# Kernel optimization log

Hardware: AMD Instinct MI355X
Metric: run time of the kernel (lower is better)

## Reference

```python
import jax, jax.numpy as jnp
import numpy as np

B, S, E, H = 4096, 200, 64, 128
V_U0, V_U1, V_I = 100000, 1000, 1000000

def setup_inputs() -> dict:
    key = jax.random.key(0)
    ks = jax.random.split(key, 16)
    s = 0.05
    return {
        'user_features': jax.random.randint(ks[0], (B, 2), 0, V_U1, dtype=jnp.int32),
        'target_item_features': jax.random.randint(ks[1], (B, 1), 0, V_I, dtype=jnp.int32),
        'behavior_sequence': jax.random.randint(ks[2], (B, S, 1), 0, V_I, dtype=jnp.int32),
        'emb_user0': jax.random.normal(ks[3], (V_U0, E), jnp.float32) * s,
        'emb_user1': jax.random.normal(ks[4], (V_U1, E), jnp.float32) * s,
        'emb_item': jax.random.normal(ks[5], (V_I, E), jnp.float32) * s,
        'att_w1': jax.random.normal(ks[6], (4 * E, H), jnp.float32) * s,
        'att_b1': jnp.zeros((H,), jnp.float32),
        'att_w2': jax.random.normal(ks[7], (H, 1), jnp.float32) * s,
        'att_b2': jnp.zeros((1,), jnp.float32),
        'fc_w1': jax.random.normal(ks[8], (4 * E, H), jnp.float32) * s,
        'fc_b1': jnp.zeros((H,), jnp.float32),
        'fc_w2': jax.random.normal(ks[9], (H, 1), jnp.float32) * s,
        'fc_b2': jnp.zeros((1,), jnp.float32),
    }

def reference(user_features, target_item_features, behavior_sequence,
              emb_user0, emb_user1, emb_item,
              att_w1, att_b1, att_w2, att_b2,
              fc_w1, fc_b1, fc_w2, fc_b2):
    # embedding gathers
    user_embeds = jnp.concatenate([emb_user0[user_features[:, 0]],
                                   emb_user1[user_features[:, 1]]], axis=-1)  # [B, 2E]
    target = emb_item[target_item_features[:, 0]]                              # [B, E]
    behavior = emb_item[behavior_sequence[:, :, 0]]                            # [B, S, E]
    t = target[:, None, :]                                                     # [B, 1, E]
    t_exp = jnp.broadcast_to(t, behavior.shape)
    att_in = jnp.concatenate([behavior, t_exp, behavior - t, behavior * t], axis=-1)  # [B, S, 4E]
    # attention MLP -> scores
    h = jax.nn.relu(jnp.einsum('bsd,dh->bsh', att_in, att_w1) + att_b1)
    scores = (jnp.einsum('bsh,ho->bso', h, att_w2) + att_b2)[..., 0]           # [B, S]
    weights = jax.nn.softmax(scores, axis=1)
    user_interest = jnp.einsum('bse,bs->be', behavior, weights)                # [B, E]
    combined = jnp.concatenate([user_embeds, user_interest, target], axis=-1)  # [B, 4E]
    out = jax.nn.relu(combined @ fc_w1 + fc_b1) @ fc_w2 + fc_b2                # [B, 1]
    return out
```

## Files before the change

### kernel.cpp

```cpp
#include <hip/hip_runtime.h>
#include <math.h>


#define S_LEN 200
#define S_PAD 208

typedef __attribute__((ext_vector_type(8))) short short8;
typedef __attribute__((ext_vector_type(4))) float f32x4;

__device__ __forceinline__ unsigned short f2b(float f) {
  union { float f; unsigned u; } x; x.f = f;
  unsigned r = x.u + 0x7fffu + ((x.u >> 16) & 1u);
  return (unsigned short)(r >> 16);
}
__device__ __forceinline__ float b2f(unsigned short h) {
  union { unsigned u; float f; } x; x.u = ((unsigned)h) << 16; return x.f;
}
__device__ __forceinline__ unsigned cvt_pk_bf16(float lo, float hi) {
  unsigned r;
  asm("v_cvt_pk_bf16_f32 %0, %1, %2" : "=v"(r) : "v"(lo), "v"(hi));
  return r;
}

__device__ __forceinline__ int swzB(int row, int col) {
  int byte = row * 128 + col * 2;
  byte ^= (row & 7) << 4;
  return byte >> 1;
}
__device__ __forceinline__ int swzW(int row, int col) {
  int byte = row * 512 + col * 2;
  byte ^= (row & 7) << 4;
  return byte >> 1;
}

__device__ __forceinline__ void async_g2l_16(const void* g, void* l) {
  __builtin_amdgcn_global_load_lds(
      (const __attribute__((address_space(1))) void*)g,
      (__attribute__((address_space(3))) void*)l, 16, 0, 0);
}

template <int CTRL>
__device__ __forceinline__ float dpp_add(float v) {
  const int t = __builtin_amdgcn_mov_dpp(__float_as_int(v), CTRL, 0xF, 0xF, true);
  return v + __int_as_float(t);
}
__device__ __forceinline__ float rowReduce16(float v) {
  v = dpp_add<0xB1>(v);
  v = dpp_add<0x4E>(v);
  v = dpp_add<0x124>(v);
  v = dpp_add<0x128>(v);
  return v;
}
__device__ __forceinline__ float permAdd16(float p) {
  float a = p, b = p;
  asm("v_permlane16_swap_b32 %0, %1" : "+v"(a), "+v"(b));
  return a + b;
}
__device__ __forceinline__ float permAdd32(float p) {
  float a = p, b = p;
  asm("v_permlane32_swap_b32 %0, %1" : "+v"(a), "+v"(b));
  return a + b;
}
__device__ __forceinline__ float waveSum64(float v) {
  return permAdd32(permAdd16(rowReduce16(v)));
}

#define WS_COMB 0
#define WS_AT   2097152
#define WS_DT   2113536
#define WS_BM   2129920
#define WS_FW1T 2146304

__global__ __launch_bounds__(256)
void din_prep(const float* __restrict__ aw1, const float* __restrict__ fw1,
              char* __restrict__ ws)
{
  unsigned short* ATc  = (unsigned short*)(ws + WS_AT);
  unsigned short* DTc  = (unsigned short*)(ws + WS_DT);
  unsigned short* BMc  = (unsigned short*)(ws + WS_BM);
  unsigned short* FW1T = (unsigned short*)(ws + WS_FW1T);
  const int blk = blockIdx.x, tid = threadIdx.x;

  if (blk < 64) {
    const int i = (blk & 31) * 256 + tid;
    const int h = i >> 6, d = i & 63;
    const int hg = h >> 5, ht = (h >> 4) & 1, hl = h & 15;
    const int kk = d >> 5, rq = (d >> 3) & 3, j = d & 7;
    const int o = (hg * 2 + ht) * 1024 + kk * 512 + rq * 128 + hl * 8 + j;
    if (blk < 32) {
      const float a  = aw1[d * 128 + h];
      const float c  = aw1[(128 + d) * 128 + h];
      const float dd = aw1[(192 + d) * 128 + h];
      ATc[o] = f2b(a + c);
      DTc[o] = f2b(dd);
    } else {
      BMc[o] = f2b(aw1[(64 + d) * 128 + h] - aw1[(128 + d) * 128 + h]);
    }
  } else {
    const int i = (blk - 64) * 256 + tid;
    const int o = 2 * i;
    const int h = o >> 9;
    const int rr = o & 511;
    const int d = (rr ^ ((h & 7) << 4)) >> 1;
    FW1T[i] = f2b(fw1[d * 128 + h]);
  }
}

__global__ __launch_bounds__(256, 4)
void din_main(const int* __restrict__ uf, const int* __restrict__ tif,
              const int* __restrict__ bseq,
              const float* __restrict__ e0, const float* __restrict__ e1,
              const float* __restrict__ ei,
              const float* __restrict__ ab1, const float* __restrict__ aw2,
              char* __restrict__ ws)
{
  __shared__ unsigned short sBeh[13312];
  __shared__ float sPart[4][S_PAD];
  __shared__ float sScores[S_PAD];
  __shared__ float sPool[4][64];
  __shared__ float sRedS[4];

  unsigned short* combS = (unsigned short*)(ws + WS_COMB);
  const unsigned short* ATc = (const unsigned short*)(ws + WS_AT);
  const unsigned short* DTc = (const unsigned short*)(ws + WS_DT);
  const unsigned short* BMc = (const unsigned short*)(ws + WS_BM);

  const int b    = blockIdx.x;
  const int tid  = threadIdx.x;
  const int lane = tid & 63;
  const int wv   = tid >> 6;
  const int hl   = lane & 15;
  const int rq   = lane >> 4;

  const int ti = tif[b];

  float4 gv[13];
#pragma unroll
  for (int it = 0; it < 13; ++it) {
    const int row = it * 16 + (tid >> 4);
    if (row < S_LEN) {
      const int idx = bseq[b * S_LEN + row];
      gv[it] = *(const float4*)(ei + (size_t)idx * 64 + (tid & 15) * 4);
    }
  }
  const float* trow = ei + (size_t)ti * 64;
  const float4 tx0 = *(const float4*)(trow + rq * 8);
  const float4 tx1 = *(const float4*)(trow + rq * 8 + 4);
  const float4 ty0 = *(const float4*)(trow + 32 + rq * 8);
  const float4 ty1 = *(const float4*)(trow + 32 + rq * 8 + 4);
  __builtin_amdgcn_sched_barrier(0);

  if (tid < 128) {
    const int row = 200 + (tid >> 4), c = (tid & 15) * 4;
    ushort4 z = {0, 0, 0, 0};
    *(ushort4*)&sBeh[swzB(row, c)] = z;
  }

  {
    unsigned short* ct = combS + (size_t)(b >> 4) * 4096;
    const int row = b & 15;
    if (tid < 64) {
      const int u0 = uf[2 * b];
      ct[swzW(row, tid)] = f2b(e0[(size_t)u0 * 64 + tid]);
    } else if (tid < 128) {
      const int u1 = uf[2 * b + 1];
      ct[swzW(row, 64 + (tid - 64))] = f2b(e1[(size_t)u1 * 64 + (tid - 64)]);
    } else if (tid < 192) {
      ct[swzW(row, 192 + (tid - 128))] = f2b(trow[tid - 128]);
    }
  }

  const float4 w2v0 = *(const float4*)(aw2 + wv * 32 + rq * 4);
  const float4 w2v1 = *(const float4*)(aw2 + wv * 32 + 16 + rq * 4);
  const f32x4 abv0 = *(const f32x4*)(ab1 + wv * 32 + rq * 4);
  const f32x4 abv1 = *(const f32x4*)(ab1 + wv * 32 + 16 + rq * 4);

  const float tt0[8] = {tx0.x, tx0.y, tx0.z, tx0.w, tx1.x, tx1.y, tx1.z, tx1.w};
  const float tt1[8] = {ty0.x, ty0.y, ty0.z, ty0.w, ty1.x, ty1.y, ty1.z, ty1.w};
  short8 w[2][2];
#pragma unroll
  for (int ht = 0; ht < 2; ++ht) {
#pragma unroll
    for (int kk = 0; kk < 2; ++kk) {
      const int fo = (wv * 2 + ht) * 1024 + kk * 512 + lane * 8;
      const short8 a8 = *(const short8*)(ATc + fo);
      const short8 d8 = *(const short8*)(DTc + fo);
      const float* tk = kk ? tt1 : tt0;
      union { short8 s; unsigned u[4]; } o;
#pragma unroll
      for (int p = 0; p < 4; ++p) {
        const float lo = fmaf(tk[2*p],   b2f((unsigned short)d8[2*p]),   b2f((unsigned short)a8[2*p]));
        const float hi = fmaf(tk[2*p+1], b2f((unsigned short)d8[2*p+1]), b2f((unsigned short)a8[2*p+1]));
        o.u[p] = cvt_pk_bf16(lo, hi);
      }
      w[ht][kk] = o.s;
    }
  }
  short8 ttB0, ttB1;
  {
    union { short8 s; unsigned u[4]; } o;
#pragma unroll
    for (int p = 0; p < 4; ++p) o.u[p] = cvt_pk_bf16(tt0[2*p], tt0[2*p+1]);
    ttB0 = o.s;
#pragma unroll
    for (int p = 0; p < 4; ++p) o.u[p] = cvt_pk_bf16(tt1[2*p], tt1[2*p+1]);
    ttB1 = o.s;
  }

#pragma unroll
  for (int it = 0; it < 13; ++it) {
    const int row = it * 16 + (tid >> 4);
    if (row < S_LEN) {
      const float4 v = gv[it];
      uint2 pk;
      pk.x = cvt_pk_bf16(v.x, v.y);
      pk.y = cvt_pk_bf16(v.z, v.w);
      *(uint2*)&sBeh[swzB(row, (tid & 15) * 4)] = pk;
    }
  }

  f32x4 accInit0, accInit1;
  {
    const f32x4 z = {0.f, 0.f, 0.f, 0.f};
    f32x4 c0 = z, c1 = z;
    const short8 bm00 = *(const short8*)(BMc + (wv * 2) * 1024 + lane * 8);
    const short8 bm01 = *(const short8*)(BMc + (wv * 2) * 1024 + 512 + lane * 8);
    const short8 bm10 = *(const short8*)(BMc + (wv * 2 + 1) * 1024 + lane * 8);
    const short8 bm11 = *(const short8*)(BMc + (wv * 2 + 1) * 1024 + 512 + lane * 8);
    c0 = __builtin_amdgcn_mfma_f32_16x16x32_bf16(bm00, ttB0, c0, 0, 0, 0);
    c0 = __builtin_amdgcn_mfma_f32_16x16x32_bf16(bm01, ttB1, c0, 0, 0, 0);
    c1 = __builtin_amdgcn_mfma_f32_16x16x32_bf16(bm10, ttB0, c1, 0, 0, 0);
    c1 = __builtin_amdgcn_mfma_f32_16x16x32_bf16(bm11, ttB1, c1, 0, 0, 0);
#pragma unroll
    for (int r = 0; r < 4; ++r) {
      accInit0[r] = c0[r] + abv0[r];
      accInit1[r] = c1[r] + abv1[r];
    }
  }
  __syncthreads();

#pragma unroll 2
  for (int tile = 0; tile < 13; ++tile) {
    const short8 av0 = *(const short8*)&sBeh[swzB(tile * 16 + hl, rq * 8)];
    const short8 av1 = *(const short8*)&sBeh[swzB(tile * 16 + hl, 32 + rq * 8)];
    f32x4 acc = accInit0;
    acc = __builtin_amdgcn_mfma_f32_16x16x32_bf16(w[0][0], av0, acc, 0, 0, 0);
    acc = __builtin_amdgcn_mfma_f32_16x16x32_bf16(w[0][1], av1, acc, 0, 0, 0);
    float p;
    p = fmaxf(acc[0], 0.f) * w2v0.x;
    p = fmaf(fmaxf(acc[1], 0.f), w2v0.y, p);
    p = fmaf(fmaxf(acc[2], 0.f), w2v0.z, p);
    p = fmaf(fmaxf(acc[3], 0.f), w2v0.w, p);
    f32x4 acc2 = accInit1;
    acc2 = __builtin_amdgcn_mfma_f32_16x16x32_bf16(w[1][0], av0, acc2, 0, 0, 0);
    acc2 = __builtin_amdgcn_mfma_f32_16x16x32_bf16(w[1][1], av1, acc2, 0, 0, 0);
    p = fmaf(fmaxf(acc2[0], 0.f), w2v1.x, p);
    p = fmaf(fmaxf(acc2[1], 0.f), w2v1.y, p);
    p = fmaf(fmaxf(acc2[2], 0.f), w2v1.z, p);
    p = fmaf(fmaxf(acc2[3], 0.f), w2v1.w, p);
    p = permAdd32(permAdd16(p));
    if (lane < 16) sPart[wv][tile * 16 + lane] = p;
  }
  __syncthreads();

  float e = 0.f;
  if (tid < S_PAD) {
    if (tid < S_LEN)
      e = __expf((sPart[0][tid] + sPart[1][tid]) + (sPart[2][tid] + sPart[3][tid]));
    sScores[tid] = e;
  }
  {
    const float s = waveSum64(e);
    if (lane == 0) sRedS[wv] = s;
  }
  __syncthreads();

  const float invS = 1.f / (sRedS[0] + sRedS[1] + sRedS[2] + sRedS[3]);

  {
    const int e2 = lane & 31, rr = lane >> 5;
    float p0 = 0.f, p1 = 0.f;
#pragma unroll
    for (int k = 0; k < 13; ++k) {
      const int base = 16 * k + 4 * wv + 2 * rr;
      const float2 sc2 = *(const float2*)&sScores[base];
      const unsigned u0 = *(const unsigned*)&sBeh[swzB(base, e2 * 2)];
      p0 = fmaf(sc2.x, __int_as_float((int)(u0 << 16)), p0);
      p1 = fmaf(sc2.x, __int_as_float((int)(u0 & 0xffff0000u)), p1);
      const unsigned u1 = *(const unsigned*)&sBeh[swzB(base + 1, e2 * 2)];
      p0 = fmaf(sc2.y, __int_as_float((int)(u1 << 16)), p0);
      p1 = fmaf(sc2.y, __int_as_float((int)(u1 & 0xffff0000u)), p1);
    }
    p0 = permAdd32(p0);
    p1 = permAdd32(p1);
    if (lane < 32) {
      float2 pr; pr.x = p0; pr.y = p1;
      *(float2*)&sPool[wv][e2 * 2] = pr;
    }
  }
  __syncthreads();

  if (tid < 64) {
    const float a = sPool[0][tid] + sPool[1][tid] + sPool[2][tid] + sPool[3][tid];
    combS[(size_t)(b >> 4) * 4096 + swzW(b & 15, 128 + tid)] = f2b(a * invS);
  }
}

__global__ __launch_bounds__(256, 2)
void din_fc(const float* __restrict__ fb1, const float* __restrict__ fw2,
            const float* __restrict__ fb2, const char* __restrict__ ws,
            float* __restrict__ out)
{
  __shared__ unsigned short sW[32768];
  __shared__ unsigned short sA[4096];
  __shared__ float sO[64];

  const int tid  = threadIdx.x;
  const int lane = tid & 63;
  const int wv   = tid >> 6;
  const int bb   = blockIdx.x * 16;

  {
    const char* srcW = ws + WS_FW1T;
    char* dstW = (char*)sW;
#pragma unroll
    for (int it = 0; it < 16; ++it)
      async_g2l_16(srcW + it * 4096 + tid * 16, dstW + it * 4096 + tid * 16);
    const char* srcA = ws + WS_COMB + (size_t)blockIdx.x * 8192;
    char* dstA = (char*)sA;
    async_g2l_16(srcA + tid * 16, dstA + tid * 16);
    async_g2l_16(srcA + 4096 + tid * 16, dstA + 4096 + tid * 16);
  }
  __syncthreads();

  const int hl = lane & 15, rq = lane >> 4;
  const int h0 = wv * 32 + hl, h1 = h0 + 16;
  f32x4 acc0 = {0.f, 0.f, 0.f, 0.f};
  f32x4 acc1 = {0.f, 0.f, 0.f, 0.f};
#pragma unroll
  for (int kk = 0; kk < 8; ++kk) {
    const short8 av = *(const short8*)&sA[swzW(hl, kk * 32 + rq * 8)];
    const short8 b0 = *(const short8*)&sW[swzW(h0, kk * 32 + rq * 8)];
    const short8 b1 = *(const short8*)&sW[swzW(h1, kk * 32 + rq * 8)];
    acc0 = __builtin_amdgcn_mfma_f32_16x16x32_bf16(av, b0, acc0, 0, 0, 0);
    acc1 = __builtin_amdgcn_mfma_f32_16x16x32_bf16(av, b1, acc1, 0, 0, 0);
  }
  const float fb10 = fb1[h0], fb11 = fb1[h1];
  const float fw20 = fw2[h0], fw21 = fw2[h1];
#pragma unroll
  for (int r = 0; r < 4; ++r) {
    float v = fmaxf(acc0[r] + fb10, 0.f) * fw20
            + fmaxf(acc1[r] + fb11, 0.f) * fw21;
    v += __shfl_xor(v, 1, 64);
    v += __shfl_xor(v, 2, 64);
    v += __shfl_xor(v, 4, 64);
    v += __shfl_xor(v, 8, 64);
    if (hl == 0) sO[wv * 16 + rq * 4 + r] = v;
  }
  __syncthreads();
  if (tid < 16)
    out[bb + tid] = sO[tid] + sO[16 + tid] + sO[32 + tid] + sO[48 + tid] + fb2[0];
}

extern "C" void kernel_launch(void* const* d_in, const int* in_sizes, int n_in,
                              void* d_out, int out_size, void* d_ws, size_t ws_size,
                              hipStream_t stream) {
  const int*   uf   = (const int*)d_in[0];
  const int*   tif  = (const int*)d_in[1];
  const int*   bseq = (const int*)d_in[2];
  const float* e0   = (const float*)d_in[3];
  const float* e1   = (const float*)d_in[4];
  const float* ei   = (const float*)d_in[5];
  const float* aw1  = (const float*)d_in[6];
  const float* ab1  = (const float*)d_in[7];
  const float* aw2  = (const float*)d_in[8];
  const float* fw1  = (const float*)d_in[10];
  const float* fb1  = (const float*)d_in[11];
  const float* fw2  = (const float*)d_in[12];
  const float* fb2  = (const float*)d_in[13];
  float* o = (float*)d_out;
  char* ws = (char*)d_ws;

  din_prep<<<dim3(192), dim3(256), 0, stream>>>(aw1, fw1, ws);
  din_main<<<dim3(4096), dim3(256), 0, stream>>>(uf, tif, bseq, e0, e1, ei,
                                                 ab1, aw2, ws);
  din_fc<<<dim3(256), dim3(256), 0, stream>>>(fb1, fw2, fb2, ws, o);
}
```

Baseline: 62.74 us.

## Fuse final FC MLP into main attention kernel, dropping separate FC launch

The separate din_fc kernel is removed. Each din_main block now computes its own row's final MLP from a shared-memory combined vector using scalar bf16 dot products against a transposed FC weight in the workspace. This saves one kernel launch and the global round trip of the combined activations. In exchange, every block reads the full 64 KB FC weight (served mostly from L2) and does the 256x128 matvec on scalar FMAs instead of batched MFMA, which adds per-block latency and extra barriers.

```diff
diff --git a/kernel.cpp b/kernel.cpp
--- a/kernel.cpp
+++ b/kernel.cpp
@@ -26,17 +26,6 @@
   int byte = row * 128 + col * 2;
   byte ^= (row & 7) << 4;
   return byte >> 1;
-}
-__device__ __forceinline__ int swzW(int row, int col) {
-  int byte = row * 512 + col * 2;
-  byte ^= (row & 7) << 4;
-  return byte >> 1;
-}
-
-__device__ __forceinline__ void async_g2l_16(const void* g, void* l) {
-  __builtin_amdgcn_global_load_lds(
-      (const __attribute__((address_space(1))) void*)g,
-      (__attribute__((address_space(3))) void*)l, 16, 0, 0);
 }
 
 template <int CTRL>
@@ -65,11 +54,10 @@
   return permAdd32(permAdd16(rowReduce16(v)));
 }
 
-#define WS_COMB 0
-#define WS_AT   2097152
-#define WS_DT   2113536
-#define WS_BM   2129920
-#define WS_FW1T 2146304
+#define WS_AT   0
+#define WS_DT   16384
+#define WS_BM   32768
+#define WS_FW1T 49152
 
 __global__ __launch_bounds__(256)
 void din_prep(const float* __restrict__ aw1, const float* __restrict__ fw1,
@@ -78,7 +66,7 @@
   unsigned short* ATc  = (unsigned short*)(ws + WS_AT);
   unsigned short* DTc  = (unsigned short*)(ws + WS_DT);
   unsigned short* BMc  = (unsigned short*)(ws + WS_BM);
-  unsigned short* FW1T = (unsigned short*)(ws + WS_FW1T);
+  unsigned short* FW1t = (unsigned short*)(ws + WS_FW1T);
   const int blk = blockIdx.x, tid = threadIdx.x;
 
   if (blk < 64) {
@@ -98,11 +86,8 @@
     }
   } else {
     const int i = (blk - 64) * 256 + tid;
-    const int o = 2 * i;
-    const int h = o >> 9;
-    const int rr = o & 511;
-    const int d = (rr ^ ((h & 7) << 4)) >> 1;
-    FW1T[i] = f2b(fw1[d * 128 + h]);
+    const int h = i >> 8, k = i & 255;
+    FW1t[i] = f2b(fw1[k * 128 + h]);
   }
 }
 
@@ -112,18 +97,22 @@
               const float* __restrict__ e0, const float* __restrict__ e1,
               const float* __restrict__ ei,
               const float* __restrict__ ab1, const float* __restrict__ aw2,
-              char* __restrict__ ws)
+              const float* __restrict__ fb1, const float* __restrict__ fw2,
+              const float* __restrict__ fb2,
+              const char* __restrict__ ws, float* __restrict__ out)
 {
   __shared__ unsigned short sBeh[13312];
   __shared__ float sPart[4][S_PAD];
   __shared__ float sScores[S_PAD];
   __shared__ float sPool[4][64];
+  __shared__ __align__(16) unsigned short sCombB[256];
+  __shared__ float sH1[256];
   __shared__ float sRedS[4];
 
-  unsigned short* combS = (unsigned short*)(ws + WS_COMB);
-  const unsigned short* ATc = (const unsigned short*)(ws + WS_AT);
-  const unsigned short* DTc = (const unsigned short*)(ws + WS_DT);
-  const unsigned short* BMc = (const unsigned short*)(ws + WS_BM);
+  const unsigned short* ATc  = (const unsigned short*)(ws + WS_AT);
+  const unsigned short* DTc  = (const unsigned short*)(ws + WS_DT);
+  const unsigned short* BMc  = (const unsigned short*)(ws + WS_BM);
+  const unsigned short* FW1t = (const unsigned short*)(ws + WS_FW1T);
 
   const int b    = blockIdx.x;
   const int tid  = threadIdx.x;
@@ -148,26 +137,22 @@
   const float4 tx1 = *(const float4*)(trow + rq * 8 + 4);
   const float4 ty0 = *(const float4*)(trow + 32 + rq * 8);
   const float4 ty1 = *(const float4*)(trow + 32 + rq * 8 + 4);
+  float combv = 0.f;
+  if (tid < 64) {
+    const int u0 = uf[2 * b];
+    combv = e0[(size_t)u0 * 64 + tid];
+  } else if (tid < 128) {
+    const int u1 = uf[2 * b + 1];
+    combv = e1[(size_t)u1 * 64 + (tid - 64)];
+  } else if (tid < 192) {
+    combv = trow[tid - 128];
+  }
   __builtin_amdgcn_sched_barrier(0);
 
   if (tid < 128) {
     const int row = 200 + (tid >> 4), c = (tid & 15) * 4;
     ushort4 z = {0, 0, 0, 0};
     *(ushort4*)&sBeh[swzB(row, c)] = z;
-  }
-
-  {
-    unsigned short* ct = combS + (size_t)(b >> 4) * 4096;
-    const int row = b & 15;
-    if (tid < 64) {
-      const int u0 = uf[2 * b];
-      ct[swzW(row, tid)] = f2b(e0[(size_t)u0 * 64 + tid]);
-    } else if (tid < 128) {
-      const int u1 = uf[2 * b + 1];
-      ct[swzW(row, 64 + (tid - 64))] = f2b(e1[(size_t)u1 * 64 + (tid - 64)]);
-    } else if (tid < 192) {
-      ct[swzW(row, 192 + (tid - 128))] = f2b(trow[tid - 128]);
-    }
   }
 
   const float4 w2v0 = *(const float4*)(aw2 + wv * 32 + rq * 4);
@@ -277,6 +262,10 @@
 
   const float invS = 1.f / (sRedS[0] + sRedS[1] + sRedS[2] + sRedS[3]);
 
+  if (tid < 64)        sCombB[tid] = f2b(combv);
+  else if (tid < 128)  sCombB[tid] = f2b(combv);
+  else if (tid < 192)  sCombB[64 + tid] = f2b(combv);
+
   {
     const int e2 = lane & 31, rr = lane >> 5;
     float p0 = 0.f, p1 = 0.f;
@@ -302,64 +291,36 @@
 
   if (tid < 64) {
     const float a = sPool[0][tid] + sPool[1][tid] + sPool[2][tid] + sPool[3][tid];
-    combS[(size_t)(b >> 4) * 4096 + swzW(b & 15, 128 + tid)] = f2b(a * invS);
-  }
-}
-
-__global__ __launch_bounds__(256, 2)
-void din_fc(const float* __restrict__ fb1, const float* __restrict__ fw2,
-            const float* __restrict__ fb2, const char* __restrict__ ws,
-            float* __restrict__ out)
-{
-  __shared__ unsigned short sW[32768];
-  __shared__ unsigned short sA[4096];
-  __shared__ float sO[64];
-
-  const int tid  = threadIdx.x;
-  const int lane = tid & 63;
-  const int wv   = tid >> 6;
-  const int bb   = blockIdx.x * 16;
-
-  {
-    const char* srcW = ws + WS_FW1T;
-    char* dstW = (char*)sW;
-#pragma unroll
-    for (int it = 0; it < 16; ++it)
-      async_g2l_16(srcW + it * 4096 + tid * 16, dstW + it * 4096 + tid * 16);
-    const char* srcA = ws + WS_COMB + (size_t)blockIdx.x * 8192;
-    char* dstA = (char*)sA;
-    async_g2l_16(srcA + tid * 16, dstA + tid * 16);
-    async_g2l_16(srcA + 4096 + tid * 16, dstA + 4096 + tid * 16);
-  }
-  __syncthreads();
-
-  const int hl = lane & 15, rq = lane >> 4;
-  const int h0 = wv * 32 + hl, h1 = h0 + 16;
-  f32x4 acc0 = {0.f, 0.f, 0.f, 0.f};
-  f32x4 acc1 = {0.f, 0.f, 0.f, 0.f};
-#pragma unroll
-  for (int kk = 0; kk < 8; ++kk) {
-    const short8 av = *(const short8*)&sA[swzW(hl, kk * 32 + rq * 8)];
-    const short8 b0 = *(const short8*)&sW[swzW(h0, kk * 32 + rq * 8)];
-    const short8 b1 = *(const short8*)&sW[swzW(h1, kk * 32 + rq * 8)];
-    acc0 = __builtin_amdgcn_mfma_f32_16x16x32_bf16(av, b0, acc0, 0, 0, 0);
-    acc1 = __builtin_amdgcn_mfma_f32_16x16x32_bf16(av, b1, acc1, 0, 0, 0);
-  }
-  const float fb10 = fb1[h0], fb11 = fb1[h1];
-  const float fw20 = fw2[h0], fw21 = fw2[h1];
-#pragma unroll
-  for (int r = 0; r < 4; ++r) {
-    float v = fmaxf(acc0[r] + fb10, 0.f) * fw20
-            + fmaxf(acc1[r] + fb11, 0.f) * fw21;
-    v += __shfl_xor(v, 1, 64);
-    v += __shfl_xor(v, 2, 64);
-    v += __shfl_xor(v, 4, 64);
-    v += __shfl_xor(v, 8, 64);
-    if (hl == 0) sO[wv * 16 + rq * 4 + r] = v;
-  }
-  __syncthreads();
-  if (tid < 16)
-    out[bb + tid] = sO[tid] + sO[16 + tid] + sO[32 + tid] + sO[48 + tid] + fb2[0];
+    sCombB[128 + tid] = f2b(a * invS);
+  }
+  __syncthreads();
+
+  {
+    const int h = tid & 127, half = tid >> 7;
+    const unsigned short* fr = FW1t + h * 256 + half * 128;
+    float acc = 0.f;
+#pragma unroll
+    for (int c8 = 0; c8 < 16; ++c8) {
+      const short8 cb = *(const short8*)&sCombB[half * 128 + c8 * 8];
+      const short8 fw = *(const short8*)(fr + c8 * 8);
+#pragma unroll
+      for (int j = 0; j < 8; ++j)
+        acc = fmaf(b2f((unsigned short)cb[j]), b2f((unsigned short)fw[j]), acc);
+    }
+    sH1[half * 128 + h] = acc;
+  }
+  __syncthreads();
+
+  if (tid < 128) {
+    const float tot = sH1[tid] + sH1[128 + tid] + fb1[tid];
+    float v = fmaxf(tot, 0.f) * fw2[tid];
+    v = waveSum64(v);
+    if (lane == 0) sRedS[wv] = v;
+  }
+  __syncthreads();
+
+  if (tid == 0)
+    out[b] = sRedS[0] + sRedS[1] + fb2[0];
 }
 
 extern "C" void kernel_launch(void* const* d_in, const int* in_sizes, int n_in,
@@ -383,6 +344,5 @@
 
   din_prep<<<dim3(192), dim3(256), 0, stream>>>(aw1, fw1, ws);
   din_main<<<dim3(4096), dim3(256), 0, stream>>>(uf, tif, bseq, e0, e1, ei,
-                                                 ab1, aw2, ws);
-  din_fc<<<dim3(256), dim3(256), 0, stream>>>(fb1, fw2, fb2, ws, o);
-}
+                                                 ab1, aw2, fb1, fw2, fb2, ws, o);
+}
```

Result: slower. 91.29 us (+45.5%).
